# Kernel optimization log

Measured on AMD Instinct MI355X. Metric: run time of the kernel, lower is better.

The kernel has to match this reference:

```python
import jax, jax.numpy as jnp
import numpy as np

DIM = 768
HEADS = 12
MAX_SEQ = 2048
F = 64  # low-rank factor; MAX_SEQ // F = 32


def setup_inputs() -> dict:
    key = jax.random.key(0)
    ks = jax.random.split(key, 6)
    s = 0.02
    x = jax.random.normal(ks[0], (4, 2048, DIM), dtype=jnp.float32)
    Wa = jax.random.normal(ks[1], (DIM, HEADS * F), dtype=jnp.float32) * s
    Wb = jax.random.normal(ks[2], (DIM, HEADS * (MAX_SEQ // F)), dtype=jnp.float32) * s
    Wv = jax.random.normal(ks[3], (DIM, DIM), dtype=jnp.float32) * s
    Wp = jax.random.normal(ks[4], (DIM, DIM), dtype=jnp.float32) * s
    bp = jnp.zeros((DIM,), dtype=jnp.float32)
    return {"x": x, "Wa": Wa, "Wb": Wb, "Wv": Wv, "Wp": Wp, "bp": bp}


def reference(x, Wa, Wb, Wv, Wp, bp):
    B, N, C = x.shape
    H, f, L = HEADS, F, MAX_SEQ
    hd = C // H
    # low-rank factors: a [B,H,N,f], b [B,H,N,L//f]
    a = (x @ Wa).reshape(B, N, H, f).transpose(0, 2, 1, 3)
    b = (x @ Wb).reshape(B, N, H, L // f).transpose(0, 2, 1, 3)
    # factorized dense scores [B,H,N,L]: a[j // (L//f)] * b[j // f]
    attn = jnp.repeat(a, L // f, axis=-1) * jnp.repeat(b, f, axis=-1)
    attn = attn[..., :N]
    attn = jax.nn.softmax(attn, axis=-1)
    v = (x @ Wv).reshape(B, N, H, hd).transpose(0, 2, 1, 3)  # [B,H,N,hd]
    out = attn @ v  # [B,H,N,hd]
    out = out.transpose(0, 2, 1, 3).reshape(B, N, C)
    return out @ Wp + bp
```

## Files before the change

kernel.cpp:

```cpp
#include <hip/hip_runtime.h>
#include <hip/hip_bf16.h>
#include <cstddef>

#define DIMC   768
#define HEADS  12
#define BATCH  4
#define SEQ    2048
#define MROWS  (BATCH * SEQ)
#define NCAT   1920
#define NAB    1152

typedef unsigned short u16;
typedef __attribute__((ext_vector_type(8))) short short8;
typedef __attribute__((ext_vector_type(4))) float floatx4;

__device__ inline u16 f2bf(float f) {
    union { float f; unsigned u; } v; v.f = f;
    unsigned u = v.u + 0x7FFF + ((v.u >> 16) & 1);
    return (u16)(u >> 16);
}
__device__ inline float bf2f(u16 h) {
    union { unsigned u; float f; } v; v.u = ((unsigned)h) << 16;
    return v.f;
}

__device__ inline void async_load16(const void* g, void* l) {
    __builtin_amdgcn_global_load_lds(
        (const __attribute__((address_space(1))) void*)g,
        (__attribute__((address_space(3))) void*)l, 16, 0, 0);
}

__global__ __launch_bounds__(256)
void prep_kernel(const float* __restrict__ x,
                 const float* __restrict__ Wa, const float* __restrict__ Wb,
                 const float* __restrict__ Wv, const float* __restrict__ Wp,
                 u16* __restrict__ xb, u16* __restrict__ Wtcat,
                 u16* __restrict__ Wpt, u16* __restrict__ xs)
{
    const int tid = threadIdx.x;
    const int bidg = blockIdx.x;
    if (bidg < 3072) {
        int i = bidg * 256 + tid;
        const float4 f0 = ((const float4*)x)[(size_t)i * 2];
        const float4 f1 = ((const float4*)x)[(size_t)i * 2 + 1];
        u16 tmp[8] = { f2bf(f0.x), f2bf(f0.y), f2bf(f0.z), f2bf(f0.w),
                       f2bf(f1.x), f2bf(f1.y), f2bf(f1.z), f2bf(f1.w) };
        *(uint4*)&xb[(size_t)i * 8] = *(uint4*)tmp;
        return;
    }
    if (bidg >= 3576) {
        const int p = bidg - 3576;
#pragma unroll
        for (int k = 0; k < 3; ++k) {
            const int c = k * 256 + tid;
            const float* src = x + (size_t)p * 32 * DIMC + c;
            float s = 0.f;
#pragma unroll
            for (int j = 0; j < 32; ++j) s += src[(size_t)j * DIMC];
            xs[(size_t)p * DIMC + c] = f2bf(s);
        }
        return;
    }
    __shared__ u16 tile[64 * 72];
    int bid = bidg - 3072;
    const float* src; u16* dst; int n0, k0, ld, col0;
    if (bid < 360) {
        int nt = bid / 12, kt = bid % 12;
        n0 = nt * 64; k0 = kt * 64; dst = Wtcat;
        if (n0 < 768)       { src = Wa; ld = 768; col0 = n0; }
        else if (n0 < 1152) { src = Wb; ld = 384; col0 = n0 - 768; }
        else                { src = Wv; ld = 768; col0 = n0 - 1152; }
    } else {
        int b2 = bid - 360;
        int nt = b2 / 12, kt = b2 % 12;
        n0 = nt * 64; k0 = kt * 64; dst = Wpt; src = Wp; ld = 768; col0 = n0;
    }
#pragma unroll
    for (int p = 0; p < 16; ++p) {
        int i = p * 256 + tid;
        int k = i >> 6, n = i & 63;
        tile[n * 72 + k] = f2bf(src[(size_t)(k0 + k) * ld + col0 + n]);
    }
    __syncthreads();
    int n = tid >> 2, kc = (tid & 3) * 16;
    uint4 o0 = *(uint4*)&tile[n * 72 + kc];
    uint4 o1 = *(uint4*)&tile[n * 72 + kc + 8];
    *(uint4*)&dst[(size_t)(n0 + n) * DIMC + k0 + kc] = o0;
    *(uint4*)&dst[(size_t)(n0 + n) * DIMC + k0 + kc + 8] = o1;
}

template<bool WRITE_BF16>
__global__ __launch_bounds__(256)
void gemm_bf16_kernel(const u16* __restrict__ A, const u16* __restrict__ Bt,
                      const float* __restrict__ bias, void* __restrict__ Cout,
                      int K, int ldC)
{
    __shared__ u16 As[2][4096];
    __shared__ u16 Bs[2][4096];

    const int tid  = threadIdx.x;
    const int lane = tid & 63, wave = tid >> 6;
    const int quad = lane >> 4, l16 = lane & 15;
    const int wm = (wave & 1) * 64, wn = (wave >> 1) * 64;
    const int m0 = blockIdx.x * 128, n0 = blockIdx.y * 128;

    const int lrow = lane >> 2, lchunk = lane & 3;
    const u16* gA = A  + (size_t)(m0 + wave * 32 + lrow) * K + lchunk * 8;
    const u16* gB = Bt + (size_t)(n0 + wave * 32 + lrow) * K + lchunk * 8;
    const int NT = K / 32;

#define STAGE(buf, kt_) do {                                                  \
        const int _k0 = (kt_) * 32;                                           \
        async_load16(gA + _k0,          &As[buf][wave * 1024]);               \
        async_load16(gA + _k0 + 16 * K, &As[buf][wave * 1024 + 512]);         \
        async_load16(gB + _k0,          &Bs[buf][wave * 1024]);               \
        async_load16(gB + _k0 + 16 * K, &Bs[buf][wave * 1024 + 512]);         \
    } while (0)

#define COMPUTE(buf) do {                                                     \
        short8 af[4], bf[4];                                                  \
        _Pragma("unroll")                                                     \
        for (int t = 0; t < 4; ++t) {                                         \
            af[t] = *(short8*)&As[buf][(wm + t * 16 + l16) * 32 + quad * 8];  \
            bf[t] = *(short8*)&Bs[buf][(wn + t * 16 + l16) * 32 + quad * 8];  \
        }                                                                     \
        _Pragma("unroll")                                                     \
        for (int mt = 0; mt < 4; ++mt)                                        \
            _Pragma("unroll")                                                 \
            for (int nt = 0; nt < 4; ++nt)                                    \
                acc[mt][nt] = __builtin_amdgcn_mfma_f32_16x16x32_bf16(        \
                    af[mt], bf[nt], acc[mt][nt], 0, 0, 0);                    \
    } while (0)

    floatx4 acc[4][4] = {};
    STAGE(0, 0);
    STAGE(1, 1);
#pragma unroll 2
    for (int kt = 0; kt < NT; ++kt) {
        const int buf = kt & 1;
        __asm__ volatile("s_waitcnt vmcnt(4)" ::: "memory");
        __asm__ volatile("s_barrier" ::: "memory");
        COMPUTE(buf);
        __asm__ volatile("s_barrier" ::: "memory");
        STAGE(buf, (kt + 2) % NT);
    }
#undef STAGE
#undef COMPUTE

#pragma unroll
    for (int mt = 0; mt < 4; ++mt)
#pragma unroll
        for (int nt = 0; nt < 4; ++nt) {
            const int gc = n0 + wn + nt * 16 + l16;
            const float bv = bias ? bias[gc] : 0.f;
#pragma unroll
            for (int r = 0; r < 4; ++r) {
                const int gr = m0 + wm + mt * 16 + quad * 4 + r;
                const float v = acc[mt][nt][r] + bv;
                if (WRITE_BF16) ((u16*)Cout)[(size_t)gr * ldC + gc] = f2bf(v);
                else            ((float*)Cout)[(size_t)gr * ldC + gc] = v;
            }
        }
}

__global__ __launch_bounds__(256)
void vs_kernel(const u16* __restrict__ xs, const u16* __restrict__ Wvt,
               u16* __restrict__ VsT)
{
    const int tid = threadIdx.x;
    const int lane = tid & 63, wave = tid >> 6;
    const int quad = lane >> 4, l16 = lane & 15;
    const int bh = blockIdx.x;
    const int b = bh / HEADS, h = bh % HEADS;
    const int K = DIMC;

    const u16* gA = Wvt + (size_t)(h * 64 + wave * 16 + l16) * K + quad * 8;
    const u16* gB = xs  + (size_t)(b * 64 + l16) * K + quad * 8;

    floatx4 acc[4] = {};
    for (int it = 0; it < 24; ++it) {
        short8 af = *(const short8*)(gA + it * 32);
        short8 bf[4];
#pragma unroll
        for (int nt = 0; nt < 4; ++nt)
            bf[nt] = *(const short8*)(gB + (size_t)nt * 16 * K + it * 32);
#pragma unroll
        for (int nt = 0; nt < 4; ++nt)
            acc[nt] = __builtin_amdgcn_mfma_f32_16x16x32_bf16(
                af, bf[nt], acc[nt], 0, 0, 0);
    }
#pragma unroll
    for (int nt = 0; nt < 4; ++nt)
#pragma unroll
        for (int r = 0; r < 4; ++r) {
            const int d = wave * 16 + quad * 4 + r;
            const int t = nt * 16 + l16;
            VsT[(size_t)bh * 4096 + d * 64 + t] = f2bf(acc[nt][r]);
        }
}

__global__ __launch_bounds__(256)
void attn_kernel(const u16* __restrict__ Yab, const u16* __restrict__ VsT,
                 u16* __restrict__ Hb)
{
    __shared__ u16 wlds[4][16 * 72];
    const int bh = blockIdx.x;
    const int h = bh % HEADS, b = bh / HEADS;
    const int tid = threadIdx.x;
    const int lane = tid & 63, wave = tid >> 6;
    const int quad = lane >> 4, l16 = lane & 15;

    const u16* vbase = VsT + (size_t)bh * 4096;
    short8 bfrag[4][2];
#pragma unroll
    for (int nt = 0; nt < 4; ++nt)
#pragma unroll
        for (int kk = 0; kk < 2; ++kk)
            bfrag[nt][kk] = *(const short8*)
                &vbase[(nt * 16 + l16) * 64 + kk * 32 + quad * 8];

    const int i0 = blockIdx.y * 64 + wave * 16;
    const u16* yrow = Yab + (size_t)(b * SEQ + i0) * NAB;
    u16* wp = &wlds[wave][0];

#pragma unroll
    for (int r = 0; r < 16; ++r) {
        float aval = bf2f(yrow[(size_t)r * NAB + h * 64 + lane]);
        float bval = bf2f(yrow[(size_t)r * NAB + 768 + h * 32 + (lane >> 1)]);
        wp[r * 72 + lane] = f2bf(__expf(aval * bval));
    }

    short8 af0 = *(short8*)&wp[l16 * 72 + quad * 8];
    short8 af1 = *(short8*)&wp[l16 * 72 + 32 + quad * 8];

    short8 ones;
#pragma unroll
    for (int j = 0; j < 8; ++j) ones[j] = (short)0x3F80;

    floatx4 acc[4] = {};
    floatx4 sacc = {};
#pragma unroll
    for (int nt = 0; nt < 4; ++nt) {
        acc[nt] = __builtin_amdgcn_mfma_f32_16x16x32_bf16(af0, bfrag[nt][0], acc[nt], 0, 0, 0);
        acc[nt] = __builtin_amdgcn_mfma_f32_16x16x32_bf16(af1, bfrag[nt][1], acc[nt], 0, 0, 0);
    }
    sacc = __builtin_amdgcn_mfma_f32_16x16x32_bf16(af0, ones, sacc, 0, 0, 0);
    sacc = __builtin_amdgcn_mfma_f32_16x16x32_bf16(af1, ones, sacc, 0, 0, 0);

    float inv[4];
#pragma unroll
    for (int r = 0; r < 4; ++r) inv[r] = 1.0f / (32.0f * sacc[r]);

#pragma unroll
    for (int nt = 0; nt < 4; ++nt)
#pragma unroll
        for (int rr = 0; rr < 4; ++rr) {
            const size_t row = (size_t)(b * SEQ + i0 + quad * 4 + rr);
            Hb[row * DIMC + h * 64 + nt * 16 + l16] = f2bf(acc[nt][rr] * inv[rr]);
        }
}

extern "C" void kernel_launch(void* const* d_in, const int* in_sizes, int n_in,
                              void* d_out, int out_size, void* d_ws, size_t ws_size,
                              hipStream_t stream)
{
    const float* x  = (const float*)d_in[0];
    const float* Wa = (const float*)d_in[1];
    const float* Wb = (const float*)d_in[2];
    const float* Wv = (const float*)d_in[3];
    const float* Wp = (const float*)d_in[4];
    const float* bp = (const float*)d_in[5];
    float* out = (float*)d_out;

    char* ws = (char*)d_ws;
    u16*   xb    = (u16*)ws;   ws += (size_t)MROWS * DIMC * 2;
    u16*   Wtcat = (u16*)ws;   ws += (size_t)NCAT * DIMC * 2;
    u16*   Wpt   = (u16*)ws;   ws += (size_t)DIMC * DIMC * 2;
    u16*   xs    = (u16*)ws;   ws += (size_t)256 * DIMC * 2;
    u16*   Yab   = (u16*)ws;   ws += (size_t)MROWS * NAB * 2;
    u16*   VsT   = (u16*)ws;   ws += (size_t)48 * 4096 * 2;
    u16*   Hb    = (u16*)ws;

    dim3 blk(256);

    prep_kernel<<<dim3(3832), blk, 0, stream>>>(x, Wa, Wb, Wv, Wp,
                                                xb, Wtcat, Wpt, xs);

    vs_kernel<<<dim3(48), blk, 0, stream>>>(xs, Wtcat + (size_t)NAB * DIMC, VsT);

    gemm_bf16_kernel<true><<<dim3(MROWS / 128, NAB / 128), blk, 0, stream>>>(
        xb, Wtcat, nullptr, Yab, DIMC, NAB);

    attn_kernel<<<dim3(BATCH * HEADS, SEQ / 64), blk, 0, stream>>>(Yab, VsT, Hb);

    gemm_bf16_kernel<false><<<dim3(MROWS / 128, DIMC / 128), blk, 0, stream>>>(
        Hb, Wpt, bp, out, DIMC, DIMC);
}
```

Baseline: 160.7 us.

## Fuse a/b projection GEMM with factorized attention to drop Yab round trip

The Wa/Wb weight rows are interleaved per head (64 a-columns followed by 32 b-columns) so that one 128x192 GEMM tile holds complete a and b factors for two heads. The new fused kernel computes that tile with MFMA and then, still in registers and LDS, forms exp(a*b), its row sums and the product with V. This removes the separate GEMM launch and the write and re-read of the bf16 Yab intermediate. In exchange the fused kernel has higher register pressure (a 4x6 accumulator tile plus V fragments) and a larger shared-memory footprint, which may lower occupancy.

```diff
diff --git a/kernel.cpp b/kernel.cpp
--- a/kernel.cpp
+++ b/kernel.cpp
@@ -64,11 +64,12 @@
     __shared__ u16 tile[64 * 72];
     int bid = bidg - 3072;
     const float* src; u16* dst; int n0, k0, ld, col0;
+    bool remap = false;
     if (bid < 360) {
         int nt = bid / 12, kt = bid % 12;
         n0 = nt * 64; k0 = kt * 64; dst = Wtcat;
-        if (n0 < 768)       { src = Wa; ld = 768; col0 = n0; }
-        else if (n0 < 1152) { src = Wb; ld = 384; col0 = n0 - 768; }
+        if (n0 < 768)       { src = Wa; ld = 768; col0 = n0; remap = true; }
+        else if (n0 < 1152) { src = Wb; ld = 384; col0 = n0 - 768; remap = true; }
         else                { src = Wv; ld = 768; col0 = n0 - 1152; }
     } else {
         int b2 = bid - 360;
@@ -83,10 +84,16 @@
     }
     __syncthreads();
     int n = tid >> 2, kc = (tid & 3) * 16;
+    int orow = n0 + n;
+    int drow = orow;
+    if (remap) {
+        if (orow < 768) drow = (orow >> 6) * 96 + (orow & 63);
+        else { int c = orow - 768; drow = (c >> 5) * 96 + 64 + (c & 31); }
+    }
     uint4 o0 = *(uint4*)&tile[n * 72 + kc];
     uint4 o1 = *(uint4*)&tile[n * 72 + kc + 8];
-    *(uint4*)&dst[(size_t)(n0 + n) * DIMC + k0 + kc] = o0;
-    *(uint4*)&dst[(size_t)(n0 + n) * DIMC + k0 + kc + 8] = o1;
+    *(uint4*)&dst[(size_t)drow * DIMC + k0 + kc] = o0;
+    *(uint4*)&dst[(size_t)drow * DIMC + k0 + kc + 8] = o1;
 }
 
 template<bool WRITE_BF16>
@@ -200,64 +207,130 @@
 }
 
 __global__ __launch_bounds__(256)
-void attn_kernel(const u16* __restrict__ Yab, const u16* __restrict__ VsT,
-                 u16* __restrict__ Hb)
-{
-    __shared__ u16 wlds[4][16 * 72];
-    const int bh = blockIdx.x;
-    const int h = bh % HEADS, b = bh / HEADS;
-    const int tid = threadIdx.x;
+void gemm1_attn_kernel(const u16* __restrict__ xb, const u16* __restrict__ Wab,
+                       const u16* __restrict__ VsT, u16* __restrict__ Hb)
+{
+    __shared__ u16 smem[20480];
+
+    const int tid  = threadIdx.x;
     const int lane = tid & 63, wave = tid >> 6;
     const int quad = lane >> 4, l16 = lane & 15;
-
-    const u16* vbase = VsT + (size_t)bh * 4096;
-    short8 bfrag[4][2];
-#pragma unroll
-    for (int nt = 0; nt < 4; ++nt)
+    const int wm = (wave & 1) * 64;
+    const int wn = (wave >> 1) * 96;
+    const int m0 = blockIdx.x * 128, n0 = blockIdx.y * 192;
+    const int K = DIMC;
+    const int NT = K / 32;
+
+    const int lrow = lane >> 2, lchunk = lane & 3;
+    const u16* gA = xb  + (size_t)(m0 + wave * 32 + lrow) * K + lchunk * 8;
+    const u16* gB = Wab + (size_t)(n0 + wave * 48 + lrow) * K + lchunk * 8;
+
+#define STAGE(buf, kt_) do {                                                  \
+        const int _k0 = (kt_) * 32;                                           \
+        u16* _as = smem + (buf) * 4096 + wave * 1024;                         \
+        u16* _bs = smem + 8192 + (buf) * 6144 + wave * 1536;                  \
+        async_load16(gA + _k0,          _as);                                 \
+        async_load16(gA + _k0 + 16 * K, _as + 512);                           \
+        async_load16(gB + _k0,          _bs);                                 \
+        async_load16(gB + _k0 + 16 * K, _bs + 512);                           \
+        async_load16(gB + _k0 + 32 * K, _bs + 1024);                          \
+    } while (0)
+
+#define COMPUTE(buf) do {                                                     \
+        const u16* _as = smem + (buf) * 4096;                                 \
+        const u16* _bs = smem + 8192 + (buf) * 6144;                          \
+        short8 af[4], bfr[6];                                                 \
+        _Pragma("unroll")                                                     \
+        for (int t = 0; t < 4; ++t)                                           \
+            af[t] = *(const short8*)&_as[(wm + t * 16 + l16) * 32 + quad * 8];\
+        _Pragma("unroll")                                                     \
+        for (int t = 0; t < 6; ++t)                                           \
+            bfr[t] = *(const short8*)&_bs[(wn + t * 16 + l16) * 32 + quad * 8];\
+        _Pragma("unroll")                                                     \
+        for (int mt = 0; mt < 4; ++mt)                                        \
+            _Pragma("unroll")                                                 \
+            for (int ct = 0; ct < 6; ++ct)                                    \
+                acc[mt][ct] = __builtin_amdgcn_mfma_f32_16x16x32_bf16(        \
+                    af[mt], bfr[ct], acc[mt][ct], 0, 0, 0);                   \
+    } while (0)
+
+    floatx4 acc[4][6] = {};
+    STAGE(0, 0);
+    STAGE(1, 1);
+#pragma unroll 2
+    for (int kt = 0; kt < NT - 2; ++kt) {
+        const int buf = kt & 1;
+        __asm__ volatile("s_waitcnt vmcnt(5)" ::: "memory");
+        __asm__ volatile("s_barrier" ::: "memory");
+        COMPUTE(buf);
+        __asm__ volatile("s_barrier" ::: "memory");
+        STAGE(buf, kt + 2);
+    }
+    __asm__ volatile("s_waitcnt vmcnt(5)" ::: "memory");
+    __asm__ volatile("s_barrier" ::: "memory");
+    COMPUTE(0);
+    __asm__ volatile("s_waitcnt vmcnt(0)" ::: "memory");
+    __asm__ volatile("s_barrier" ::: "memory");
+    COMPUTE(1);
+    __syncthreads();
+#undef STAGE
+#undef COMPUTE
+
+    const int b = blockIdx.x >> 4;
+    const int h = blockIdx.y * 2 + (wave >> 1);
+    const u16* vbase = VsT + ((size_t)b * HEADS + h) * 4096;
+
+    short8 bV[4][2];
+#pragma unroll
+    for (int nt2 = 0; nt2 < 4; ++nt2)
 #pragma unroll
         for (int kk = 0; kk < 2; ++kk)
-            bfrag[nt][kk] = *(const short8*)
-                &vbase[(nt * 16 + l16) * 64 + kk * 32 + quad * 8];
-
-    const int i0 = blockIdx.y * 64 + wave * 16;
-    const u16* yrow = Yab + (size_t)(b * SEQ + i0) * NAB;
-    u16* wp = &wlds[wave][0];
-
-#pragma unroll
-    for (int r = 0; r < 16; ++r) {
-        float aval = bf2f(yrow[(size_t)r * NAB + h * 64 + lane]);
-        float bval = bf2f(yrow[(size_t)r * NAB + 768 + h * 32 + (lane >> 1)]);
-        wp[r * 72 + lane] = f2bf(__expf(aval * bval));
-    }
-
-    short8 af0 = *(short8*)&wp[l16 * 72 + quad * 8];
-    short8 af1 = *(short8*)&wp[l16 * 72 + 32 + quad * 8];
+            bV[nt2][kk] = *(const short8*)
+                &vbase[(nt2 * 16 + l16) * 64 + kk * 32 + quad * 8];
+
+    u16* Pw = smem + wave * 4608;
+    const int srcl0 = quad * 16 + (l16 >> 1);
+    const int srcl1 = srcl0 + 8;
 
     short8 ones;
 #pragma unroll
     for (int j = 0; j < 8; ++j) ones[j] = (short)0x3F80;
 
-    floatx4 acc[4] = {};
-    floatx4 sacc = {};
-#pragma unroll
-    for (int nt = 0; nt < 4; ++nt) {
-        acc[nt] = __builtin_amdgcn_mfma_f32_16x16x32_bf16(af0, bfrag[nt][0], acc[nt], 0, 0, 0);
-        acc[nt] = __builtin_amdgcn_mfma_f32_16x16x32_bf16(af1, bfrag[nt][1], acc[nt], 0, 0, 0);
-    }
-    sacc = __builtin_amdgcn_mfma_f32_16x16x32_bf16(af0, ones, sacc, 0, 0, 0);
-    sacc = __builtin_amdgcn_mfma_f32_16x16x32_bf16(af1, ones, sacc, 0, 0, 0);
-
-    float inv[4];
-#pragma unroll
-    for (int r = 0; r < 4; ++r) inv[r] = 1.0f / (32.0f * sacc[r]);
-
-#pragma unroll
-    for (int nt = 0; nt < 4; ++nt)
-#pragma unroll
-        for (int rr = 0; rr < 4; ++rr) {
-            const size_t row = (size_t)(b * SEQ + i0 + quad * 4 + rr);
-            Hb[row * DIMC + h * 64 + nt * 16 + l16] = f2bf(acc[nt][rr] * inv[rr]);
-        }
+#pragma unroll
+    for (int mt = 0; mt < 4; ++mt) {
+#pragma unroll
+        for (int nt = 0; nt < 4; ++nt) {
+            const int src = (nt & 1) ? srcl1 : srcl0;
+#pragma unroll
+            for (int r = 0; r < 4; ++r) {
+                float bsh = __shfl(acc[mt][4 + (nt >> 1)][r], src, 64);
+                float e = __expf(acc[mt][nt][r] * bsh);
+                Pw[(mt * 16 + quad * 4 + r) * 72 + nt * 16 + l16] = f2bf(e);
+            }
+        }
+        short8 a0 = *(const short8*)&Pw[(mt * 16 + l16) * 72 + quad * 8];
+        short8 a1 = *(const short8*)&Pw[(mt * 16 + l16) * 72 + 32 + quad * 8];
+        floatx4 sacc = {};
+        sacc = __builtin_amdgcn_mfma_f32_16x16x32_bf16(a0, ones, sacc, 0, 0, 0);
+        sacc = __builtin_amdgcn_mfma_f32_16x16x32_bf16(a1, ones, sacc, 0, 0, 0);
+        floatx4 accO[4] = {};
+#pragma unroll
+        for (int nt2 = 0; nt2 < 4; ++nt2) {
+            accO[nt2] = __builtin_amdgcn_mfma_f32_16x16x32_bf16(a0, bV[nt2][0], accO[nt2], 0, 0, 0);
+            accO[nt2] = __builtin_amdgcn_mfma_f32_16x16x32_bf16(a1, bV[nt2][1], accO[nt2], 0, 0, 0);
+        }
+        float inv[4];
+#pragma unroll
+        for (int r = 0; r < 4; ++r) inv[r] = 1.0f / (32.0f * sacc[r]);
+#pragma unroll
+        for (int nt2 = 0; nt2 < 4; ++nt2)
+#pragma unroll
+            for (int rr = 0; rr < 4; ++rr) {
+                const size_t row = (size_t)(m0 + wm + mt * 16 + quad * 4 + rr);
+                Hb[row * DIMC + h * 64 + nt2 * 16 + l16] =
+                    f2bf(accO[nt2][rr] * inv[rr]);
+            }
+    }
 }
 
 extern "C" void kernel_launch(void* const* d_in, const int* in_sizes, int n_in,
@@ -277,7 +350,6 @@
     u16*   Wtcat = (u16*)ws;   ws += (size_t)NCAT * DIMC * 2;
     u16*   Wpt   = (u16*)ws;   ws += (size_t)DIMC * DIMC * 2;
     u16*   xs    = (u16*)ws;   ws += (size_t)256 * DIMC * 2;
-    u16*   Yab   = (u16*)ws;   ws += (size_t)MROWS * NAB * 2;
     u16*   VsT   = (u16*)ws;   ws += (size_t)48 * 4096 * 2;
     u16*   Hb    = (u16*)ws;
 
@@ -288,10 +360,8 @@
 
     vs_kernel<<<dim3(48), blk, 0, stream>>>(xs, Wtcat + (size_t)NAB * DIMC, VsT);
 
-    gemm_bf16_kernel<true><<<dim3(MROWS / 128, NAB / 128), blk, 0, stream>>>(
-        xb, Wtcat, nullptr, Yab, DIMC, NAB);
-
-    attn_kernel<<<dim3(BATCH * HEADS, SEQ / 64), blk, 0, stream>>>(Yab, VsT, Hb);
+    gemm1_attn_kernel<<<dim3(MROWS / 128, NAB / 192), blk, 0, stream>>>(
+        xb, Wtcat, VsT, Hb);
 
     gemm_bf16_kernel<false><<<dim3(MROWS / 128, DIMC / 128), blk, 0, stream>>>(
         Hb, Wpt, bp, out, DIMC, DIMC);
```

Result: no change. 160.1 us (-0.3%).
